# Kernel optimization log

Measured on AMD Instinct MI355X. Metric: run time of the kernel, lower is better.

The kernel has to match this reference:

```python
import jax, jax.numpy as jnp
import numpy as np
import math

B, S, D, H, L, F, V, C = 8, 1024, 768, 12, 6, 3072, 32000, 10
DK = D // H
EPS = 1e-5


def _pos_encoding(seq_len, d):
    pos = jnp.arange(seq_len, dtype=jnp.float32)[:, None]
    div = jnp.exp(jnp.arange(0, d, 2, dtype=jnp.float32) * (-math.log(10000.0) / d))
    pe = jnp.zeros((seq_len, d), dtype=jnp.float32)
    pe = pe.at[:, 0::2].set(jnp.sin(pos * div))
    pe = pe.at[:, 1::2].set(jnp.cos(pos * div))
    return pe


def _layernorm(x, scale, bias):
    mu = jnp.mean(x, axis=-1, keepdims=True)
    var = jnp.mean(jnp.square(x - mu), axis=-1, keepdims=True)
    return (x - mu) * jax.lax.rsqrt(var + EPS) * scale + bias


def setup_inputs() -> dict:
    key = jax.random.key(0)
    ks = jax.random.split(key, 14)
    s = 0.02
    return {
        "tokens": jax.random.randint(ks[0], (B, S), 0, V),
        "emb": jax.random.normal(ks[1], (V, D), jnp.float32) * s,
        "Wq": jax.random.normal(ks[2], (L, D, D), jnp.float32) * s,
        "Wk": jax.random.normal(ks[3], (L, D, D), jnp.float32) * s,
        "Wv": jax.random.normal(ks[4], (L, D, D), jnp.float32) * s,
        "Wo": jax.random.normal(ks[5], (L, D, D), jnp.float32) * s,
        "W1": jax.random.normal(ks[6], (L, D, F), jnp.float32) * s,
        "W2": jax.random.normal(ks[7], (L, F, D), jnp.float32) * s,
        "ln1_s": jnp.ones((L, D), jnp.float32),
        "ln1_b": jnp.zeros((L, D), jnp.float32),
        "ln2_s": jnp.ones((L, D), jnp.float32),
        "ln2_b": jnp.zeros((L, D), jnp.float32),
        "Wc": jax.random.normal(ks[8], (D, C), jnp.float32) * s,
        "bc": jnp.zeros((C,), jnp.float32),
    }


def _block(x, p):
    Wq, Wk, Wv, Wo, W1, W2, l1s, l1b, l2s, l2b = p
    b, s = x.shape[0], x.shape[1]
    q = (x @ Wq).reshape(b, s, H, DK)
    k = (x @ Wk).reshape(b, s, H, DK)
    v = (x @ Wv).reshape(b, s, H, DK)
    scores = jnp.einsum("bqhd,bkhd->bhqk", q, k) / math.sqrt(DK)
    attn = jax.nn.softmax(scores, axis=-1)
    out = jnp.einsum("bhqk,bkhd->bqhd", attn, v).reshape(b, s, D) @ Wo
    x = _layernorm(x + out, l1s, l1b)
    ffn = jax.nn.relu(x @ W1) @ W2
    x = _layernorm(x + ffn, l2s, l2b)
    return x


def reference(tokens, emb, Wq, Wk, Wv, Wo, W1, W2, ln1_s, ln1_b, ln2_s, ln2_b, Wc, bc):
    x = emb[tokens] + _pos_encoding(tokens.shape[1], D)[None]

    def step(h, p):
        return _block(h, p), None

    x, _ = jax.lax.scan(step, x, (Wq, Wk, Wv, Wo, W1, W2, ln1_s, ln1_b, ln2_s, ln2_b))
    pooled = jnp.mean(x, axis=1)  # [B, D]
    return pooled @ Wc + bc
```

## Files before the change

kernel.cpp:

```cpp
#include <hip/hip_runtime.h>
#include <hip/hip_bf16.h>
#include <math.h>

#define BB 8
#define SS 1024
#define DD 768
#define HH 12
#define LL 6
#define FF 3072
#define CC 10
#define BS_ (BB * SS)

#define WT_STRIDE (2304 * 768 + 768 * 768 + 3072 * 768 + 768 * 3072)

typedef __attribute__((ext_vector_type(8))) short short8v;
typedef __attribute__((ext_vector_type(4))) float f32x4;
typedef __attribute__((ext_vector_type(8))) unsigned short ushort8v;
typedef __attribute__((ext_vector_type(4))) unsigned short ushort4v;
typedef __attribute__((ext_vector_type(2))) unsigned int uint2v;

#define CEXPQ 0.18033688f

__device__ inline unsigned short f2bf(float f) {
  unsigned int u = __builtin_bit_cast(unsigned int, f);
  u += 0x7fffu + ((u >> 16) & 1u);
  return (unsigned short)(u >> 16);
}
__device__ inline float bf2f(unsigned short u) {
  return __builtin_bit_cast(float, (unsigned int)u << 16);
}
__device__ inline unsigned int cvtpk(float lo, float hi) {
  unsigned int r;
  asm("v_cvt_pk_bf16_f32 %0, %1, %2" : "=v"(r) : "v"(lo), "v"(hi));
  return r;
}
__device__ inline void gload16(const void* g, void* l) {
  __builtin_amdgcn_global_load_lds((const __attribute__((address_space(1))) void*)g,
                                   (__attribute__((address_space(3))) void*)l, 16, 0, 0);
}

__device__ inline float wave_sum(float v) {
#pragma unroll
  for (int off = 32; off > 0; off >>= 1) v += __shfl_down(v, off);
  return v;
}

__global__ __launch_bounds__(256) void k_embed(const int* __restrict__ tokens,
                                               const float* __restrict__ emb,
                                               ushort* __restrict__ xb) {
  int row = blockIdx.x;
  int s = row & (SS - 1);
  int tok = tokens[row];
  const float* e = emb + (size_t)tok * DD;
  ushort* xbr = xb + (size_t)row * DD;
  for (int d = threadIdx.x; d < DD; d += 256) {
    float freq = expf((float)(d & ~1) * -0.0119926306f);
    float ang = (float)s * freq;
    float pe = (d & 1) ? cosf(ang) : sinf(ang);
    xbr[d] = f2bf(e[d] + pe);
  }
}

__global__ __launch_bounds__(256) void k_transpose_all(
    const float* __restrict__ Wq, const float* __restrict__ Wk,
    const float* __restrict__ Wv, const float* __restrict__ Wo,
    const float* __restrict__ W1, const float* __restrict__ W2,
    ushort* __restrict__ wt) {
  __shared__ float tile[32][33];
  int bid = blockIdx.x;
  int lyr = blockIdx.y;
  ushort* wqkv_t = wt + (size_t)lyr * WT_STRIDE;
  ushort* wo_t = wqkv_t + 2304 * 768;
  ushort* w1_t = wo_t + 768 * 768;
  ushort* w2_t = w1_t + 3072 * 768;
  const float* W; ushort* Wt; int K, N, lb;
  if (bid < 1728) {
    int m = bid / 576; lb = bid - m * 576;
    W = ((m == 0) ? Wq : (m == 1) ? Wk : Wv) + (size_t)lyr * DD * DD;
    Wt = wqkv_t + m * 768 * 768; K = 768; N = 768;
  } else if (bid < 2304) {
    W = Wo + (size_t)lyr * DD * DD; Wt = wo_t; K = 768; N = 768; lb = bid - 1728;
  } else if (bid < 4608) {
    W = W1 + (size_t)lyr * DD * FF; Wt = w1_t; K = 768; N = 3072; lb = bid - 2304;
  } else {
    W = W2 + (size_t)lyr * FF * DD; Wt = w2_t; K = 3072; N = 768; lb = bid - 4608;
  }
  int nbk = K >> 5;
  int k0 = (lb % nbk) * 32, n0 = (lb / nbk) * 32;
  int t = threadIdx.x;
  int r = t >> 3, c4 = (t & 7) * 4;
  float4 v = *(const float4*)(W + (size_t)(k0 + r) * N + n0 + c4);
  tile[r][c4 + 0] = v.x; tile[r][c4 + 1] = v.y;
  tile[r][c4 + 2] = v.z; tile[r][c4 + 3] = v.w;
  __syncthreads();
  ushort4v o;
#pragma unroll
  for (int i = 0; i < 4; ++i) o[i] = f2bf(tile[c4 + i][r]);
  *(ushort4v*)(Wt + (size_t)(n0 + r) * K + k0 + c4) = o;
}

template <int RELU, int TN, int SCALEQ = 0>
__global__ __launch_bounds__(256) void k_gemm_db(const ushort* __restrict__ A,
                                                 const ushort* __restrict__ Bt,
                                                 ushort* __restrict__ Cout,
                                                 int M, int N, int K) {
  constexpr int NF = TN / 32;
  __shared__ ushort smem[2][(128 + TN) * 64];
  int bidl = blockIdx.y * gridDim.x + blockIdx.x;
  int nwg = gridDim.x * gridDim.y;
  int cpx = nwg >> 3;
  int tid = (bidl & 7) * cpx + (bidl >> 3);
  int n0 = (tid % gridDim.x) * TN, m0 = (tid / gridDim.x) * 128;
  int t = threadIdx.x, w = t >> 6, l = t & 63;
  int wr = (w >> 1) * 64, wc = (w & 1) * (TN / 2);
  int lr = l & 15, lg = l >> 4;
  f32x4 acc[4][NF] = {};
  int sr8 = l >> 3;
  int scw = ((l & 7) ^ sr8) * 8;
  const ushort* ag = A + (size_t)(m0 + w * 8 + sr8) * K + scw;
  const ushort* bg = Bt + (size_t)(n0 + w * 8 + sr8) * K + scw;
  int nk = K >> 6;
  {
    ushort* al = &smem[0][(w * 8) * 64];
    ushort* bl = &smem[0][128 * 64 + (w * 8) * 64];
#pragma unroll
    for (int ii = 0; ii < 4; ++ii) gload16(ag + (size_t)ii * 32 * K, al + ii * 2048);
#pragma unroll
    for (int ii = 0; ii < TN / 32; ++ii) gload16(bg + (size_t)ii * 32 * K, bl + ii * 2048);
  }
  int rsw = lr & 7;
  for (int k = 0; k < nk; ++k) {
    __syncthreads();
    if (k + 1 < nk) {
      int kb = (k + 1) & 1;
      int kc0 = (k + 1) * 64;
      ushort* al = &smem[kb][(w * 8) * 64];
      ushort* bl = &smem[kb][128 * 64 + (w * 8) * 64];
#pragma unroll
      for (int ii = 0; ii < 4; ++ii) gload16(ag + (size_t)ii * 32 * K + kc0, al + ii * 2048);
#pragma unroll
      for (int ii = 0; ii < TN / 32; ++ii) gload16(bg + (size_t)ii * 32 * K + kc0, bl + ii * 2048);
    }
    const ushort* As = &smem[k & 1][0];
    const ushort* Bs = &smem[k & 1][128 * 64];
#pragma unroll
    for (int ks = 0; ks < 2; ++ks) {
      short8v af[4], bfr[NF];
#pragma unroll
      for (int mi = 0; mi < 4; ++mi)
        af[mi] = *(const short8v*)(As + (wr + mi * 16 + lr) * 64 + (((ks * 4 + lg) ^ rsw) << 3));
#pragma unroll
      for (int ni = 0; ni < NF; ++ni)
        bfr[ni] = *(const short8v*)(Bs + (wc + ni * 16 + lr) * 64 + (((ks * 4 + lg) ^ rsw) << 3));
      __builtin_amdgcn_s_setprio(1);
#pragma unroll
      for (int mi = 0; mi < 4; ++mi)
#pragma unroll
        for (int ni = 0; ni < NF; ++ni)
          acc[mi][ni] = __builtin_amdgcn_mfma_f32_16x16x32_bf16(af[mi], bfr[ni], acc[mi][ni], 0, 0, 0);
      __builtin_amdgcn_s_setprio(0);
    }
  }
  __syncthreads();
  float osc = (SCALEQ && n0 < 768) ? CEXPQ : 1.0f;
  ushort* cst = &smem[0][0];
#pragma unroll
  for (int mi = 0; mi < 4; ++mi)
#pragma unroll
    for (int ni = 0; ni < NF; ++ni) {
      int cl = wc + ni * 16 + lr;
#pragma unroll
      for (int i = 0; i < 4; ++i) {
        int rl = wr + mi * 16 + lg * 4 + i;
        float v = acc[mi][ni][i];
        if (RELU) v = fmaxf(v, 0.f);
        if (SCALEQ) v *= osc;
        cst[rl * TN + (cl ^ (((rl >> 2) & 3) << 4))] = f2bf(v);
      }
    }
  __syncthreads();
  {
    int row = t >> 1, half = t & 1;
    int swr = ((row >> 2) & 3) << 4;
    ushort* crow = Cout + (size_t)(m0 + row) * N + n0 + half * (TN / 2);
#pragma unroll
    for (int c8 = 0; c8 < TN / 16; ++c8) {
      int c = half * (TN / 2) + c8 * 8;
      ushort8v vv = *(const ushort8v*)(&cst[row * TN + (c ^ swr)]);
      *(ushort8v*)(crow + c8 * 8) = vv;
    }
  }
}

__global__ __launch_bounds__(256) void k_flash(const ushort* __restrict__ qkv,
                                               ushort* __restrict__ ao) {
  __shared__ ushort Ks[64][64];
  __shared__ ushort Vt[64][64];
  __shared__ ushort Ps[4][32][64];
  const int LD = 2304;
  int bidl = blockIdx.y * gridDim.x + blockIdx.x;
  int tid = (bidl & 7) * 96 + (bidl >> 3);
  int qt = tid & 7;
  int bh = tid >> 3;
  int h = bh % HH, b = bh / HH;
  int t = threadIdx.x, w = t >> 6, l = t & 63;
  int lr = l & 15, lg = l >> 4;
  int sw = (l & 7) << 3;
  int q0 = qt * 128;
  const ushort* qbase = qkv + (size_t)(b * SS) * LD + h * 64;
  const ushort* kbase = qbase + 768;
  const ushort* vbase = qbase + 1536;
  short8v qf[2][2];
#pragma unroll
  for (int qg = 0; qg < 2; ++qg) {
    const ushort* qrow = qbase + (size_t)(q0 + w * 32 + qg * 16 + lr) * LD + lg * 8;
    qf[qg][0] = *(const short8v*)(qrow);
    qf[qg][1] = *(const short8v*)(qrow + 32);
  }
  float l_run[2] = {0.f, 0.f};
  f32x4 o_acc[2][4] = {};
  int krow_ = w * 16 + (l >> 3);
  int kcol_ = ((l & 7) * 8) ^ ((krow_ & 7) << 3);
  const ushort* kg = kbase + (size_t)krow_ * LD + kcol_;
  ushort* kl = &Ks[w * 16][0];
  int d_ = t & 7;
  int dk0 = d_ * 8;
  int kv2 = (t >> 3) * 2;
  for (int kt = 0; kt < 16; ++kt) {
    int kv0 = kt * 64;
    const ushort* vr0 = vbase + (size_t)(kv0 + kv2) * LD + dk0;
    ushort8v v0 = *(const ushort8v*)(vr0);
    ushort8v v1 = *(const ushort8v*)(vr0 + LD);
    __syncthreads();
    gload16(kg + (size_t)kv0 * LD, kl);
    gload16(kg + (size_t)(kv0 + 8) * LD, kl + 512);
#pragma unroll
    for (int i = 0; i < 8; ++i) {
      unsigned int pack = (unsigned int)v0[i] | ((unsigned int)v1[i] << 16);
      *(unsigned int*)(&Vt[dk0 + i][kv2 ^ (((i ^ d_) & 7) << 3)]) = pack;
    }
    __syncthreads();
    short8v kf[4][2];
#pragma unroll
    for (int mi = 0; mi < 4; ++mi) {
      int kvr = mi * 16 + lr;
      kf[mi][0] = *(const short8v*)(&Ks[kvr][(lg * 8) ^ sw]);
      kf[mi][1] = *(const short8v*)(&Ks[kvr][(32 + lg * 8) ^ sw]);
    }
    f32x4 s[2][4] = {};
    __builtin_amdgcn_s_setprio(1);
#pragma unroll
    for (int mi = 0; mi < 4; ++mi)
#pragma unroll
      for (int qg = 0; qg < 2; ++qg) {
        s[qg][mi] = __builtin_amdgcn_mfma_f32_16x16x32_bf16(kf[mi][0], qf[qg][0], s[qg][mi], 0, 0, 0);
        s[qg][mi] = __builtin_amdgcn_mfma_f32_16x16x32_bf16(kf[mi][1], qf[qg][1], s[qg][mi], 0, 0, 0);
      }
    __builtin_amdgcn_s_setprio(0);
#pragma unroll
    for (int qg = 0; qg < 2; ++qg) {
      float psum = 0.f;
#pragma unroll
      for (int mi = 0; mi < 4; ++mi) {
        float p0 = exp2f(s[qg][mi][0]);
        float p1 = exp2f(s[qg][mi][1]);
        float p2 = exp2f(s[qg][mi][2]);
        float p3 = exp2f(s[qg][mi][3]);
        psum += (p0 + p1) + (p2 + p3);
        uint2v pp;
        pp.x = cvtpk(p0, p1);
        pp.y = cvtpk(p2, p3);
        *(uint2v*)(&Ps[w][qg * 16 + lr][(mi * 16 + lg * 4) ^ ((lr & 7) << 3)]) = pp;
      }
      psum += __shfl_xor(psum, 16);
      psum += __shfl_xor(psum, 32);
      l_run[qg] += psum;
    }
#pragma unroll
    for (int ks = 0; ks < 2; ++ks) {
      short8v pf[2];
      pf[0] = *(const short8v*)(&Ps[w][lr][(ks * 32 + lg * 8) ^ sw]);
      pf[1] = *(const short8v*)(&Ps[w][16 + lr][(ks * 32 + lg * 8) ^ sw]);
      short8v vf[4];
#pragma unroll
      for (int mi = 0; mi < 4; ++mi) {
        int swz = ((lr & 7) ^ (mi * 2 + (lr >> 3))) & 7;
        vf[mi] = *(const short8v*)(&Vt[mi * 16 + lr][(ks * 32 + lg * 8) ^ (swz << 3)]);
      }
      __builtin_amdgcn_s_setprio(1);
#pragma unroll
      for (int mi = 0; mi < 4; ++mi)
#pragma unroll
        for (int qg = 0; qg < 2; ++qg)
          o_acc[qg][mi] = __builtin_amdgcn_mfma_f32_16x16x32_bf16(vf[mi], pf[qg], o_acc[qg][mi], 0, 0, 0);
      __builtin_amdgcn_s_setprio(0);
    }
  }
#pragma unroll
  for (int qg = 0; qg < 2; ++qg) {
    float invl = 1.f / l_run[qg];
    ushort* orow = ao + (size_t)(b * SS + q0 + w * 32 + qg * 16 + lr) * DD + h * 64;
#pragma unroll
    for (int mi = 0; mi < 4; ++mi) {
      ushort4v o;
#pragma unroll
      for (int i = 0; i < 4; ++i) o[i] = f2bf(o_acc[qg][mi][i] * invl);
      *(ushort4v*)(orow + mi * 16 + lg * 4) = o;
    }
  }
}

__global__ __launch_bounds__(64) void k_addln(ushort* __restrict__ xb,
                                              const ushort* __restrict__ y,
                                              const float* __restrict__ sc,
                                              const float* __restrict__ bi) {
  int row = blockIdx.x, l = threadIdx.x;
  int d0 = l * 12;
  ushort* xr = xb + (size_t)row * DD;
  const ushort* yr = y + (size_t)row * DD;
  ushort4v xa[3], ya[3];
#pragma unroll
  for (int j = 0; j < 3; ++j) {
    xa[j] = *(const ushort4v*)(xr + d0 + j * 4);
    ya[j] = *(const ushort4v*)(yr + d0 + j * 4);
  }
  float v[12];
  float s = 0.f;
#pragma unroll
  for (int j = 0; j < 3; ++j)
#pragma unroll
    for (int i = 0; i < 4; ++i) {
      float vv = bf2f(xa[j][i]) + bf2f(ya[j][i]);
      v[j * 4 + i] = vv;
      s += vv;
    }
  float mu = wave_sum(s);
  mu = __shfl(mu, 0) * (1.f / 768.f);
  float vs = 0.f;
#pragma unroll
  for (int i = 0; i < 12; ++i) {
    float c = v[i] - mu;
    vs += c * c;
  }
  vs = wave_sum(vs);
  float rstd = rsqrtf(__shfl(vs, 0) * (1.f / 768.f) + 1e-5f);
  float4 scv[3], biv[3];
#pragma unroll
  for (int j = 0; j < 3; ++j) {
    scv[j] = *(const float4*)(sc + d0 + j * 4);
    biv[j] = *(const float4*)(bi + d0 + j * 4);
  }
#pragma unroll
  for (int j = 0; j < 3; ++j) {
    ushort4v o;
    const float* sj = (const float*)&scv[j];
    const float* bj = (const float*)&biv[j];
#pragma unroll
    for (int i = 0; i < 4; ++i) o[i] = f2bf((v[j * 4 + i] - mu) * rstd * sj[i] + bj[i]);
    *(ushort4v*)(xr + d0 + j * 4) = o;
  }
}

__global__ __launch_bounds__(256) void k_pool(const ushort* __restrict__ xb,
                                              float* __restrict__ pooled) {
  int b = blockIdx.x, chunk = blockIdx.y, t = threadIdx.x;
  float a0 = 0, a1 = 0, a2 = 0;
  for (int s2 = chunk * 128; s2 < chunk * 128 + 128; ++s2) {
    const ushort* xr = xb + (size_t)(b * SS + s2) * DD;
    a0 += bf2f(xr[t]); a1 += bf2f(xr[t + 256]); a2 += bf2f(xr[t + 512]);
  }
  atomicAdd(&pooled[b * DD + t], a0 * (1.f / 1024.f));
  atomicAdd(&pooled[b * DD + t + 256], a1 * (1.f / 1024.f));
  atomicAdd(&pooled[b * DD + t + 512], a2 * (1.f / 1024.f));
}

__global__ __launch_bounds__(64) void k_cls(const float* __restrict__ pooled,
                                            const float* __restrict__ Wc,
                                            const float* __restrict__ bc,
                                            float* __restrict__ out) {
  int idx = blockIdx.x;
  int b = idx / CC, c = idx % CC;
  int t = threadIdx.x;
  float acc = 0.f;
  for (int d0 = t; d0 < DD; d0 += 64) acc = fmaf(pooled[b * DD + d0], Wc[d0 * CC + c], acc);
  acc = wave_sum(acc);
  if (t == 0) out[b * CC + c] = acc + bc[c];
}

extern "C" void kernel_launch(void* const* d_in, const int* in_sizes, int n_in,
                              void* d_out, int out_size, void* d_ws, size_t ws_size,
                              hipStream_t stream) {
  (void)in_sizes; (void)n_in; (void)out_size; (void)ws_size;
  const int* tokens = (const int*)d_in[0];
  const float* emb = (const float*)d_in[1];
  const float* Wq = (const float*)d_in[2];
  const float* Wk = (const float*)d_in[3];
  const float* Wv = (const float*)d_in[4];
  const float* Wo = (const float*)d_in[5];
  const float* W1 = (const float*)d_in[6];
  const float* W2 = (const float*)d_in[7];
  const float* l1s = (const float*)d_in[8];
  const float* l1b = (const float*)d_in[9];
  const float* l2s = (const float*)d_in[10];
  const float* l2b = (const float*)d_in[11];
  const float* Wc = (const float*)d_in[12];
  const float* bc = (const float*)d_in[13];
  float* out = (float*)d_out;

  char* p = (char*)d_ws;
  ushort* xb = (ushort*)p;              p += (size_t)BS_ * DD * 2;
  ushort* qkvb = (ushort*)p;
  ushort* hb = (ushort*)p;
  ushort* ao = (ushort*)(p + (size_t)BS_ * 2304 * 2);
  p += (size_t)BS_ * FF * 2;
  ushort* yb = (ushort*)p;              p += (size_t)BS_ * DD * 2;
  ushort* wt = (ushort*)p;              p += (size_t)WT_STRIDE * LL * 2;
  float* pooled = (float*)p;

  k_embed<<<BS_, 256, 0, stream>>>(tokens, emb, xb);
  k_transpose_all<<<dim3(6912, LL), 256, 0, stream>>>(Wq, Wk, Wv, Wo, W1, W2, wt);

  for (int l = 0; l < LL; ++l) {
    ushort* wqkv_t = wt + (size_t)l * WT_STRIDE;
    ushort* wo_t = wqkv_t + 2304 * 768;
    ushort* w1_t = wo_t + 768 * 768;
    ushort* w2_t = w1_t + 3072 * 768;

    k_gemm_db<0, 128, 1><<<dim3(2304 / 128, BS_ / 128), 256, 0, stream>>>(xb, wqkv_t, qkvb, BS_, 2304, DD);
    k_flash<<<dim3(8, BB * HH), 256, 0, stream>>>(qkvb, ao);
    k_gemm_db<0, 64><<<dim3(DD / 64, BS_ / 128), 256, 0, stream>>>(ao, wo_t, yb, BS_, DD, DD);
    k_addln<<<BS_, 64, 0, stream>>>(xb, yb, l1s + l * DD, l1b + l * DD);
    k_gemm_db<1, 128><<<dim3(FF / 128, BS_ / 128), 256, 0, stream>>>(xb, w1_t, hb, BS_, FF, DD);
    k_gemm_db<0, 64><<<dim3(DD / 64, BS_ / 128), 256, 0, stream>>>(hb, w2_t, yb, BS_, DD, FF);
    k_addln<<<BS_, 64, 0, stream>>>(xb, yb, l2s + l * DD, l2b + l * DD);
  }

  hipMemsetAsync(pooled, 0, (size_t)BB * DD * sizeof(float), stream);
  k_pool<<<dim3(BB, 8), 256, 0, stream>>>(xb, pooled);
  k_cls<<<BB * CC, 64, 0, stream>>>(pooled, Wc, bc, out);
}
```

Before: 1.403 ms.

## Prefetch GEMM tiles two stages ahead with explicit vmcnt waits; widen transpose tiles

The GEMM main loop now issues the first two K-tiles up front. Each iteration waits on the vector-memory counter only for the current tile, loads all LDS fragments for both k-substeps, then passes a barrier before issuing the global load for tile k+2 into the buffer just consumed. This keeps a global load in flight across each iteration instead of one sync-then-load per step. Separately, the weight transpose kernel moves to 64x64 tiles with wider 16-byte bf16 stores and 4x fewer blocks. The hand-written vmcnt counts depend on the number of gload16 issues per tile, so they are fragile if the load pattern changes.

```diff
diff --git a/kernel.cpp b/kernel.cpp
--- a/kernel.cpp
+++ b/kernel.cpp
@@ -66,7 +66,7 @@
     const float* __restrict__ Wv, const float* __restrict__ Wo,
     const float* __restrict__ W1, const float* __restrict__ W2,
     ushort* __restrict__ wt) {
-  __shared__ float tile[32][33];
+  __shared__ float tile[64][65];
   int bid = blockIdx.x;
   int lyr = blockIdx.y;
   ushort* wqkv_t = wt + (size_t)lyr * WT_STRIDE;
@@ -74,29 +74,42 @@
   ushort* w1_t = wo_t + 768 * 768;
   ushort* w2_t = w1_t + 3072 * 768;
   const float* W; ushort* Wt; int K, N, lb;
-  if (bid < 1728) {
-    int m = bid / 576; lb = bid - m * 576;
+  if (bid < 432) {
+    int m = bid / 144; lb = bid - m * 144;
     W = ((m == 0) ? Wq : (m == 1) ? Wk : Wv) + (size_t)lyr * DD * DD;
     Wt = wqkv_t + m * 768 * 768; K = 768; N = 768;
-  } else if (bid < 2304) {
-    W = Wo + (size_t)lyr * DD * DD; Wt = wo_t; K = 768; N = 768; lb = bid - 1728;
-  } else if (bid < 4608) {
-    W = W1 + (size_t)lyr * DD * FF; Wt = w1_t; K = 768; N = 3072; lb = bid - 2304;
+  } else if (bid < 576) {
+    W = Wo + (size_t)lyr * DD * DD; Wt = wo_t; K = 768; N = 768; lb = bid - 432;
+  } else if (bid < 1152) {
+    W = W1 + (size_t)lyr * DD * FF; Wt = w1_t; K = 768; N = 3072; lb = bid - 576;
   } else {
-    W = W2 + (size_t)lyr * FF * DD; Wt = w2_t; K = 3072; N = 768; lb = bid - 4608;
-  }
-  int nbk = K >> 5;
-  int k0 = (lb % nbk) * 32, n0 = (lb / nbk) * 32;
+    W = W2 + (size_t)lyr * FF * DD; Wt = w2_t; K = 3072; N = 768; lb = bid - 1152;
+  }
+  int nbk = K >> 6;
+  int k0 = (lb % nbk) * 64, n0 = (lb / nbk) * 64;
   int t = threadIdx.x;
-  int r = t >> 3, c4 = (t & 7) * 4;
-  float4 v = *(const float4*)(W + (size_t)(k0 + r) * N + n0 + c4);
-  tile[r][c4 + 0] = v.x; tile[r][c4 + 1] = v.y;
-  tile[r][c4 + 2] = v.z; tile[r][c4 + 3] = v.w;
+  {
+    int r = t >> 2, cl = (t & 3) * 16;
+    const float* wrow = W + (size_t)(k0 + r) * N + n0 + cl;
+#pragma unroll
+    for (int j = 0; j < 4; ++j) {
+      float4 v = *(const float4*)(wrow + j * 4);
+      tile[r][cl + j * 4 + 0] = v.x; tile[r][cl + j * 4 + 1] = v.y;
+      tile[r][cl + j * 4 + 2] = v.z; tile[r][cl + j * 4 + 3] = v.w;
+    }
+  }
   __syncthreads();
-  ushort4v o;
-#pragma unroll
-  for (int i = 0; i < 4; ++i) o[i] = f2bf(tile[c4 + i][r]);
-  *(ushort4v*)(Wt + (size_t)(n0 + r) * K + k0 + c4) = o;
+  {
+    int n = t >> 2, cq = (t & 3) * 16;
+    ushort8v o0, o1;
+#pragma unroll
+    for (int jj = 0; jj < 8; ++jj) o0[jj] = f2bf(tile[cq + jj][n]);
+#pragma unroll
+    for (int jj = 0; jj < 8; ++jj) o1[jj] = f2bf(tile[cq + 8 + jj][n]);
+    ushort* orow = Wt + (size_t)(n0 + n) * K + k0 + cq;
+    *(ushort8v*)(orow) = o0;
+    *(ushort8v*)(orow + 8) = o1;
+  }
 }
 
 template <int RELU, int TN, int SCALEQ = 0>
@@ -120,47 +133,56 @@
   const ushort* ag = A + (size_t)(m0 + w * 8 + sr8) * K + scw;
   const ushort* bg = Bt + (size_t)(n0 + w * 8 + sr8) * K + scw;
   int nk = K >> 6;
-  {
-    ushort* al = &smem[0][(w * 8) * 64];
-    ushort* bl = &smem[0][128 * 64 + (w * 8) * 64];
-#pragma unroll
-    for (int ii = 0; ii < 4; ++ii) gload16(ag + (size_t)ii * 32 * K, al + ii * 2048);
-#pragma unroll
-    for (int ii = 0; ii < TN / 32; ++ii) gload16(bg + (size_t)ii * 32 * K, bl + ii * 2048);
-  }
+
+#define STAGE_TILE(KC0, BUF)                                                     \
+  {                                                                              \
+    ushort* al = &smem[BUF][(w * 8) * 64];                                       \
+    ushort* bl = &smem[BUF][128 * 64 + (w * 8) * 64];                            \
+    _Pragma("unroll") for (int ii = 0; ii < 4; ++ii)                             \
+        gload16(ag + (size_t)ii * 32 * K + (KC0), al + ii * 2048);               \
+    _Pragma("unroll") for (int ii = 0; ii < TN / 32; ++ii)                       \
+        gload16(bg + (size_t)ii * 32 * K + (KC0), bl + ii * 2048);               \
+  }
+
+  STAGE_TILE(0, 0);
+  if (nk > 1) STAGE_TILE(64, 1);
   int rsw = lr & 7;
   for (int k = 0; k < nk; ++k) {
-    __syncthreads();
     if (k + 1 < nk) {
-      int kb = (k + 1) & 1;
-      int kc0 = (k + 1) * 64;
-      ushort* al = &smem[kb][(w * 8) * 64];
-      ushort* bl = &smem[kb][128 * 64 + (w * 8) * 64];
-#pragma unroll
-      for (int ii = 0; ii < 4; ++ii) gload16(ag + (size_t)ii * 32 * K + kc0, al + ii * 2048);
-#pragma unroll
-      for (int ii = 0; ii < TN / 32; ++ii) gload16(bg + (size_t)ii * 32 * K + kc0, bl + ii * 2048);
-    }
+      if constexpr (TN == 128) asm volatile("s_waitcnt vmcnt(8)" ::: "memory");
+      else                     asm volatile("s_waitcnt vmcnt(6)" ::: "memory");
+    } else {
+      asm volatile("s_waitcnt vmcnt(0)" ::: "memory");
+    }
+    __builtin_amdgcn_s_barrier();
+    __builtin_amdgcn_sched_barrier(0);
     const ushort* As = &smem[k & 1][0];
     const ushort* Bs = &smem[k & 1][128 * 64];
+    short8v af[2][4], bfr[2][NF];
 #pragma unroll
     for (int ks = 0; ks < 2; ++ks) {
-      short8v af[4], bfr[NF];
 #pragma unroll
       for (int mi = 0; mi < 4; ++mi)
-        af[mi] = *(const short8v*)(As + (wr + mi * 16 + lr) * 64 + (((ks * 4 + lg) ^ rsw) << 3));
+        af[ks][mi] = *(const short8v*)(As + (wr + mi * 16 + lr) * 64 + (((ks * 4 + lg) ^ rsw) << 3));
 #pragma unroll
       for (int ni = 0; ni < NF; ++ni)
-        bfr[ni] = *(const short8v*)(Bs + (wc + ni * 16 + lr) * 64 + (((ks * 4 + lg) ^ rsw) << 3));
-      __builtin_amdgcn_s_setprio(1);
+        bfr[ks][ni] = *(const short8v*)(Bs + (wc + ni * 16 + lr) * 64 + (((ks * 4 + lg) ^ rsw) << 3));
+    }
+    asm volatile("s_waitcnt lgkmcnt(0)" ::: "memory");
+    __builtin_amdgcn_s_barrier();
+    __builtin_amdgcn_sched_barrier(0);
+    if (k + 2 < nk) STAGE_TILE((k + 2) * 64, k & 1);
+    __builtin_amdgcn_s_setprio(1);
+#pragma unroll
+    for (int ks = 0; ks < 2; ++ks)
 #pragma unroll
       for (int mi = 0; mi < 4; ++mi)
 #pragma unroll
         for (int ni = 0; ni < NF; ++ni)
-          acc[mi][ni] = __builtin_amdgcn_mfma_f32_16x16x32_bf16(af[mi], bfr[ni], acc[mi][ni], 0, 0, 0);
-      __builtin_amdgcn_s_setprio(0);
-    }
-  }
+          acc[mi][ni] = __builtin_amdgcn_mfma_f32_16x16x32_bf16(af[ks][mi], bfr[ks][ni], acc[mi][ni], 0, 0, 0);
+    __builtin_amdgcn_s_setprio(0);
+  }
+#undef STAGE_TILE
   __syncthreads();
   float osc = (SCALEQ && n0 < 768) ? CEXPQ : 1.0f;
   ushort* cst = &smem[0][0];
@@ -418,7 +440,7 @@
   float* pooled = (float*)p;
 
   k_embed<<<BS_, 256, 0, stream>>>(tokens, emb, xb);
-  k_transpose_all<<<dim3(6912, LL), 256, 0, stream>>>(Wq, Wk, Wv, Wo, W1, W2, wt);
+  k_transpose_all<<<dim3(1728, LL), 256, 0, stream>>>(Wq, Wk, Wv, Wo, W1, W2, wt);
 
   for (int l = 0; l < LL; ++l) {
     ushort* wqkv_t = wt + (size_t)l * WT_STRIDE;
```

New measurement: 1.399 ms. No clear change (-0.2%).
